# Performance work log

Measured on AMD Instinct MI355X. Metric: run time of the kernel, lower is better.

Reference implementation:

```python
import jax, jax.numpy as jnp
import numpy as np

DIM = 128      # dim
NC = 50000     # number of code nodes
NE = 100000    # number of hyperedges (visits)
T = 800000     # total flattened (code, edge) incidences
GAMMA = 0.5


def setup_inputs() -> dict:
    key = jax.random.key(0)
    ks = jax.random.split(key, 18)
    d = DIM
    s = 1.0 / np.sqrt(d)
    return {
        "H_e": jax.random.normal(ks[0], (NE, d), jnp.float32),
        "H_c": jax.random.normal(ks[1], (NC, d), jnp.float32),
        "timestamps": jax.random.uniform(ks[2], (NE,), jnp.float32),
        "W_e": jax.random.normal(ks[3], (d, d), jnp.float32) * s,
        "be_lin": jax.random.normal(ks[4], (d,), jnp.float32) * s,
        "b_e": jnp.zeros((d,), jnp.float32),
        "W_c": jax.random.normal(ks[5], (d, d), jnp.float32) * s,
        "bc_lin": jax.random.normal(ks[6], (d,), jnp.float32) * s,
        "b_c": jnp.zeros((d,), jnp.float32),
        "W_t": jax.random.normal(ks[7], (d, d), jnp.float32) * s,
        "b_t": jax.random.normal(ks[8], (d,), jnp.float32) * s,
        "W_g": jax.random.normal(ks[9], (d, d), jnp.float32) * s,
        "b_g": jax.random.normal(ks[10], (d,), jnp.float32) * s,
        "omega": jax.random.normal(ks[11], (d // 2,), jnp.float32),
        "W_t2v": jax.random.normal(ks[12], (d, d), jnp.float32) * s,
        "b_t2v": jax.random.normal(ks[13], (d,), jnp.float32) * s,
        "edge_ids": jax.random.randint(ks[14], (T,), 0, NE, jnp.int32),
        "seg_ids": jnp.sort(jax.random.randint(ks[15], (T,), 0, NC, jnp.int32)),
    }


def reference(H_e, H_c, timestamps, W_e, be_lin, b_e, W_c, bc_lin, b_c,
              W_t, b_t, W_g, b_g, omega, W_t2v, b_t2v, edge_ids, seg_ids):
    n_codes = H_c.shape[0]
    # --- gather variable-length neighbor sets (flattened segments) ---
    hes = H_e[edge_ids]                      # [T, d]
    hcs = H_c[seg_ids]                       # [T, d]
    tes = timestamps[edge_ids]               # [T]
    # --- Time2Vec ---
    tw = tes[:, None] * omega                # [T, d//2]
    t2v = jnp.concatenate([jnp.cos(tw), jnp.sin(tw)], axis=-1) @ W_t2v + b_t2v  # [T, d]
    # --- score: <proj_e * proj_c, sigmoid(linear_t(alpha_e))> ---
    proj_e = hes @ W_e + be_lin + b_e        # [T, d]
    proj_c = hcs @ W_c + bc_lin + b_c        # [T, d]
    gate = jax.nn.sigmoid(t2v @ W_t + b_t)   # [T, d]
    scores = jnp.sum(proj_e * proj_c * gate, axis=-1)  # [T]
    # --- segment softmax over each code's neighbor set ---
    smax = jax.ops.segment_max(scores, seg_ids, num_segments=n_codes)
    smax = jnp.where(jnp.isfinite(smax), smax, 0.0)
    ex = jnp.exp(scores - smax[seg_ids])
    denom = jax.ops.segment_sum(ex, seg_ids, num_segments=n_codes)
    attn = ex / jnp.maximum(denom, 1e-30)[seg_ids]      # [T]
    # --- weighted aggregate of g(h_e), scatter back to codes ---
    msg = attn[:, None] * (hes @ W_g + b_g)             # [T, d]
    agg = jax.ops.segment_sum(msg, seg_ids, num_segments=n_codes)  # [Nc, d]
    cnt = jax.ops.segment_sum(jnp.ones_like(scores), seg_ids, num_segments=n_codes)
    has_edge = (cnt > 0)[:, None]
    return jnp.where(has_edge, GAMMA * agg + (1.0 - GAMMA) * H_c, H_c)
```

## Files before the change

kernel.cpp:

```cpp
#include <hip/hip_runtime.h>
#include <math.h>

#define DIM   128
#define NC_   50000
#define NE_   100000
#define T_    800000

typedef __attribute__((ext_vector_type(8))) _Float16 f16x8;
typedef __attribute__((ext_vector_type(2))) _Float16 f16x2;
typedef __attribute__((ext_vector_type(4))) float f32x4;

__device__ __forceinline__ float sigmoidf_(float x) {
    return 1.f / (1.f + __expf(-x));
}

__device__ __forceinline__ float dot2f(f16x2 a, f16x2 b, float c) {
#if defined(__has_builtin) && __has_builtin(__builtin_amdgcn_fdot2)
    return __builtin_amdgcn_fdot2(a, b, c, false);
#else
    return c + (float)a[0] * (float)b[0] + (float)a[1] * (float)b[1];
#endif
}

__global__ __launch_bounds__(128)
void k_combine(const float* __restrict__ W_t2v, const float* __restrict__ W_t,
               const float* __restrict__ b_t2v, const float* __restrict__ b_t,
               float* __restrict__ W_tt, float* __restrict__ b_tt) {
    const int i = blockIdx.x, j = threadIdx.x;
    float acc = 0.f;
    if (i < DIM) {
        for (int k = 0; k < DIM; ++k) acc = fmaf(W_t2v[i*DIM+k], W_t[k*DIM+j], acc);
        W_tt[i*DIM+j] = acc;
    } else {
        for (int k = 0; k < DIM; ++k) acc = fmaf(b_t2v[k], W_t[k*DIM+j], acc);
        b_tt[j] = acc + b_t[j];
    }
}

__global__ __launch_bounds__(64)
void k_pack(const float* __restrict__ s0, const float* __restrict__ s1,
            const float* __restrict__ s2, const float* __restrict__ s3,
            _Float16* __restrict__ d0, _Float16* __restrict__ d1,
            _Float16* __restrict__ d2, _Float16* __restrict__ d3) {
    const float* srcs[4] = {s0, s1, s2, s3};
    _Float16* dsts[4] = {d0, d1, d2, d3};
    const float* src = srcs[blockIdx.y];
    _Float16* dst = dsts[blockIdx.y];
    const int b = blockIdx.x;
    const int nt = b >> 2, kb = b & 3;
    const int lane = threadIdx.x;
    const int n  = nt * 16 + (lane & 15);
    const int k0 = kb * 32 + 8 * (lane >> 4);
    const size_t off = ((size_t)(nt * 4 + kb) * 64 + lane) * 8;
    #pragma unroll
    for (int e = 0; e < 8; ++e)
        dst[off + e] = (_Float16)src[(size_t)(k0 + e) * DIM + n];
}

__global__ __launch_bounds__(256)
void k_starts(const int* __restrict__ seg, int* __restrict__ start) {
    int t = blockIdx.x * 256 + threadIdx.x;
    if (t > T_) return;
    if (t < T_) {
        int s  = seg[t];
        int sp = (t > 0) ? seg[t-1] : -1;
        for (int c = sp + 1; c <= s; ++c) start[c] = t;
    } else {
        int sp = seg[T_-1];
        for (int c = sp + 1; c <= NC_; ++c) start[c] = T_;
    }
}

__device__ __forceinline__ void split8h(const float* xs, f16x8* hi, f16x8* lo) {
    #pragma unroll
    for (int e = 0; e < 8; ++e) {
        _Float16 h = (_Float16)xs[e];
        (*hi)[e] = h;
        (*lo)[e] = (_Float16)(xs[e] - (float)h);
    }
}

__device__ __forceinline__ void stage_lds(_Float16* lds, const _Float16* __restrict__ g) {
    const int tid = threadIdx.x;
    #pragma unroll
    for (int i = 0; i < 8; ++i)
        ((uint4*)lds)[tid + i * 256] = ((const uint4*)g)[tid + i * 256];
}

__device__ __forceinline__ void mfma2(f16x8 ahi, f16x8 alo, const _Float16* lds_bp,
                                      f32x4* acc) {
    f16x8 b = *(const f16x8*)lds_bp;
    *acc = __builtin_amdgcn_mfma_f32_16x16x32_f16(ahi, b, *acc, 0, 0, 0);
    *acc = __builtin_amdgcn_mfma_f32_16x16x32_f16(alo, b, *acc, 0, 0, 0);
}

__global__ __launch_bounds__(256)
void k_edge(const float* __restrict__ H_e, const float* __restrict__ ts,
            const _Float16* __restrict__ packWe, const _Float16* __restrict__ packWtt,
            const float* __restrict__ be_lin, const float* __restrict__ b_e,
            const float* __restrict__ b_tt, const float* __restrict__ omega,
            _Float16* __restrict__ u16, _Float16* __restrict__ He16) {
    __shared__ __align__(16) _Float16 ldsW[16384];
    const int tid  = threadIdx.x;
    const int lane = tid & 63;
    const int q    = lane & 15, g = lane >> 4;
    const int brow = blockIdx.x * 64 + (tid >> 6) * 16;
    const int arow = brow + q;
    const bool valid = arow < NE_;
    const float* ap = H_e + (size_t)(valid ? arow : 0) * DIM;
    const float te  = valid ? ts[arow] : 0.f;

    stage_lds(ldsW, packWe);

    f32x4 accU[8], accG[8];
    #pragma unroll
    for (int i = 0; i < 8; ++i) {
        accU[i] = (f32x4){0.f, 0.f, 0.f, 0.f};
        accG[i] = (f32x4){0.f, 0.f, 0.f, 0.f};
    }
    __syncthreads();

    #pragma unroll
    for (int kb = 0; kb < 4; ++kb) {
        const int k0 = kb * 32 + 8 * g;
        float xs[8];
        if (valid) {
            float4 x0 = *(const float4*)(ap + k0);
            float4 x1 = *(const float4*)(ap + k0 + 4);
            xs[0]=x0.x; xs[1]=x0.y; xs[2]=x0.z; xs[3]=x0.w;
            xs[4]=x1.x; xs[5]=x1.y; xs[6]=x1.z; xs[7]=x1.w;
        } else {
            #pragma unroll
            for (int e = 0; e < 8; ++e) xs[e] = 0.f;
        }
        f16x8 ahi, alo;
        split8h(xs, &ahi, &alo);
        if (valid) *(f16x8*)&He16[(size_t)arow * DIM + k0] = ahi;
        #pragma unroll
        for (int nt = 0; nt < 8; ++nt)
            mfma2(ahi, alo, &ldsW[((nt * 4 + kb) * 64 + lane) * 8], &accU[nt]);
    }

    __syncthreads();
    stage_lds(ldsW, packWtt);
    __syncthreads();

    #pragma unroll
    for (int kb = 0; kb < 4; ++kb) {
        const int k0 = kb * 32 + 8 * g;
        float ys[8];
        #pragma unroll
        for (int e = 0; e < 8; ++e) {
            const int k = k0 + e;
            float x = te * omega[k & 63];
            float s, c;
            __sincosf(x, &s, &c);
            ys[e] = (k < 64) ? c : s;
        }
        f16x8 thi, tlo;
        split8h(ys, &thi, &tlo);
        #pragma unroll
        for (int nt = 0; nt < 8; ++nt)
            mfma2(thi, tlo, &ldsW[((nt * 4 + kb) * 64 + lane) * 8], &accG[nt]);
    }

    #pragma unroll
    for (int nt = 0; nt < 8; ++nt) {
        const int col = nt * 16 + q;
        const float bu = be_lin[col] + b_e[col];
        const float bg = b_tt[col];
        #pragma unroll
        for (int reg = 0; reg < 4; ++reg) {
            const int e = brow + 4 * g + reg;
            if (e < NE_) {
                float val = (accU[nt][reg] + bu) * sigmoidf_(accG[nt][reg] + bg);
                u16[(size_t)e * DIM + col] = (_Float16)val;
            }
        }
    }
}

__global__ __launch_bounds__(256)
void k_code(const float* __restrict__ H_c, const _Float16* __restrict__ packWc,
            const float* __restrict__ bc_lin, const float* __restrict__ b_c,
            _Float16* __restrict__ pc16) {
    __shared__ __align__(16) _Float16 ldsW[16384];
    const int tid  = threadIdx.x;
    const int lane = tid & 63;
    const int q    = lane & 15, g = lane >> 4;
    const int brow = blockIdx.x * 64 + (tid >> 6) * 16;
    const int arow = brow + q;
    const bool valid = arow < NC_;
    const float* ap = H_c + (size_t)(valid ? arow : 0) * DIM;

    stage_lds(ldsW, packWc);

    f32x4 acc[8];
    #pragma unroll
    for (int i = 0; i < 8; ++i) acc[i] = (f32x4){0.f, 0.f, 0.f, 0.f};
    __syncthreads();

    #pragma unroll
    for (int kb = 0; kb < 4; ++kb) {
        const int k0 = kb * 32 + 8 * g;
        float xs[8];
        if (valid) {
            float4 x0 = *(const float4*)(ap + k0);
            float4 x1 = *(const float4*)(ap + k0 + 4);
            xs[0]=x0.x; xs[1]=x0.y; xs[2]=x0.z; xs[3]=x0.w;
            xs[4]=x1.x; xs[5]=x1.y; xs[6]=x1.z; xs[7]=x1.w;
        } else {
            #pragma unroll
            for (int e = 0; e < 8; ++e) xs[e] = 0.f;
        }
        f16x8 ahi, alo;
        split8h(xs, &ahi, &alo);
        #pragma unroll
        for (int nt = 0; nt < 8; ++nt)
            mfma2(ahi, alo, &ldsW[((nt * 4 + kb) * 64 + lane) * 8], &acc[nt]);
    }

    #pragma unroll
    for (int nt = 0; nt < 8; ++nt) {
        const int col = nt * 16 + q;
        const float bc = bc_lin[col] + b_c[col];
        #pragma unroll
        for (int reg = 0; reg < 4; ++reg) {
            const int c = brow + 4 * g + reg;
            if (c < NC_) pc16[(size_t)c * DIM + col] = (_Float16)(acc[nt][reg] + bc);
        }
    }
}

__global__ __launch_bounds__(256)
void k_seg(const _Float16* __restrict__ u16, _Float16* __restrict__ pc16,
           const _Float16* __restrict__ He16, const int* __restrict__ edge_ids,
           const int* __restrict__ start) {
    const int lane = threadIdx.x & 63;
    const int c = blockIdx.x * 4 + (threadIdx.x >> 6);
    if (c >= NC_) return;
    const int lo = start[c], hi = start[c + 1];
    const int g = lane >> 3;
    const int q = lane & 7;
    const int j0 = q * 16;

    union { uint4 r[2]; f16x2 h2[8]; } pcu;
    pcu.r[0] = *(const uint4*)&pc16[(size_t)c * DIM + j0];
    pcu.r[1] = *(const uint4*)&pc16[(size_t)c * DIM + j0 + 8];

    float M = -INFINITY, S = 0.f;
    float acc[16];
    #pragma unroll
    for (int i = 0; i < 16; ++i) acc[i] = 0.f;

    for (int base = lo; base < hi; base += 64) {
        const int n = min(64, hi - base);
        const int eid = (base + lane < hi) ? edge_ids[base + lane] : 0;
        const int niter = (n + 7) >> 3;
        float msc = -INFINITY;

        for (int jj = 0; jj < niter; ++jj) {
            const int s = 8 * jj + g;
            const int e = __shfl(eid, s);
            float p = 0.f;
            if (s < n) {
                union { uint4 r[2]; f16x2 h2[8]; } uu;
                const _Float16* up = &u16[(size_t)e * DIM + j0];
                uu.r[0] = *(const uint4*)up;
                uu.r[1] = *(const uint4*)(up + 8);
                #pragma unroll
                for (int i = 0; i < 8; ++i) p = dot2f(uu.h2[i], pcu.h2[i], p);
            }
            p += __shfl_xor(p, 1);
            p += __shfl_xor(p, 2);
            p += __shfl_xor(p, 4);
            if (q == jj && s < n) msc = p;
        }

        float cm = msc;
        #pragma unroll
        for (int off = 32; off; off >>= 1) cm = fmaxf(cm, __shfl_xor(cm, off));
        const float nM = fmaxf(M, cm);
        const float scale = __expf(M - nM);
        const float pi = __expf(msc - nM);
        float ss = pi;
        #pragma unroll
        for (int off = 32; off; off >>= 1) ss += __shfl_xor(ss, off);
        S = S * scale + ss;
        #pragma unroll
        for (int i = 0; i < 16; ++i) acc[i] *= scale;
        M = nM;

        for (int jj = 0; jj < niter; ++jj) {
            const int s = 8 * jj + g;
            const int e = __shfl(eid, s);
            const float p = __shfl(pi, 8 * g + jj);
            if (s < n) {
                union { uint4 r[2]; f16x8 h8[2]; } hh;
                const _Float16* hp = &He16[(size_t)e * DIM + j0];
                hh.r[0] = *(const uint4*)hp;
                hh.r[1] = *(const uint4*)(hp + 8);
                #pragma unroll
                for (int i = 0; i < 8; ++i) {
                    acc[i]     = fmaf(p, (float)hh.h8[0][i], acc[i]);
                    acc[8 + i] = fmaf(p, (float)hh.h8[1][i], acc[8 + i]);
                }
            }
        }
    }

    #pragma unroll
    for (int off = 8; off <= 32; off <<= 1) {
        #pragma unroll
        for (int i = 0; i < 16; ++i) acc[i] += __shfl_xor(acc[i], off);
    }

    if (g == 0) {
        const float inv = (hi > lo) ? 1.f / fmaxf(S, 1e-30f) : 0.f;
        union { uint4 r[2]; _Float16 h[16]; } o;
        #pragma unroll
        for (int i = 0; i < 16; ++i) o.h[i] = (_Float16)(acc[i] * inv);
        *(uint4*)&pc16[(size_t)c * DIM + j0]     = o.r[0];
        *(uint4*)&pc16[(size_t)c * DIM + j0 + 8] = o.r[1];
    }
}

__global__ __launch_bounds__(256)
void k_out(const _Float16* __restrict__ v16, const _Float16* __restrict__ packWg,
           const float* __restrict__ b_g, const float* __restrict__ H_c,
           const int* __restrict__ start, float* __restrict__ out) {
    __shared__ __align__(16) _Float16 ldsW[16384];
    const int tid  = threadIdx.x;
    const int lane = tid & 63;
    const int q    = lane & 15, g = lane >> 4;
    const int brow = blockIdx.x * 64 + (tid >> 6) * 16;
    const int arow = brow + q;
    const bool valid = arow < NC_;
    const _Float16* ap = v16 + (size_t)(valid ? arow : 0) * DIM;

    stage_lds(ldsW, packWg);

    f32x4 acc[8];
    #pragma unroll
    for (int i = 0; i < 8; ++i) acc[i] = (f32x4){0.f, 0.f, 0.f, 0.f};
    __syncthreads();

    #pragma unroll
    for (int kb = 0; kb < 4; ++kb) {
        const int k0 = kb * 32 + 8 * g;
        f16x8 a;
        if (valid) {
            a = *(const f16x8*)(ap + k0);
        } else {
            #pragma unroll
            for (int e = 0; e < 8; ++e) a[e] = (_Float16)0.f;
        }
        #pragma unroll
        for (int nt = 0; nt < 8; ++nt) {
            f16x8 b = *(const f16x8*)&ldsW[((nt * 4 + kb) * 64 + lane) * 8];
            acc[nt] = __builtin_amdgcn_mfma_f32_16x16x32_f16(a, b, acc[nt], 0, 0, 0);
        }
    }

    #pragma unroll
    for (int reg = 0; reg < 4; ++reg) {
        const int c = brow + 4 * g + reg;
        if (c >= NC_) continue;
        const bool has = start[c + 1] > start[c];
        #pragma unroll
        for (int nt = 0; nt < 8; ++nt) {
            const int col = nt * 16 + q;
            const float hc = H_c[(size_t)c * DIM + col];
            float o = has ? 0.5f * (acc[nt][reg] + b_g[col]) + 0.5f * hc : hc;
            out[(size_t)c * DIM + col] = o;
        }
    }
}

extern "C" void kernel_launch(void* const* d_in, const int* in_sizes, int n_in,
                              void* d_out, int out_size, void* d_ws, size_t ws_size,
                              hipStream_t stream) {
    const float* H_e    = (const float*)d_in[0];
    const float* H_c    = (const float*)d_in[1];
    const float* ts     = (const float*)d_in[2];
    const float* W_e    = (const float*)d_in[3];
    const float* be_lin = (const float*)d_in[4];
    const float* b_e    = (const float*)d_in[5];
    const float* W_c    = (const float*)d_in[6];
    const float* bc_lin = (const float*)d_in[7];
    const float* b_c    = (const float*)d_in[8];
    const float* W_t    = (const float*)d_in[9];
    const float* b_t    = (const float*)d_in[10];
    const float* W_g    = (const float*)d_in[11];
    const float* b_g    = (const float*)d_in[12];
    const float* omega  = (const float*)d_in[13];
    const float* W_t2v  = (const float*)d_in[14];
    const float* b_t2v  = (const float*)d_in[15];
    const int* edge_ids = (const int*)d_in[16];
    const int* seg_ids  = (const int*)d_in[17];
    float* out = (float*)d_out;

    char* w = (char*)d_ws;
    _Float16* u16  = (_Float16*)w; w += (size_t)NE_ * DIM * sizeof(_Float16);
    _Float16* He16 = (_Float16*)w; w += (size_t)NE_ * DIM * sizeof(_Float16);
    _Float16* pc16 = (_Float16*)w; w += (size_t)NC_ * DIM * sizeof(_Float16);
    int* start  = (int*)w;    w += (((size_t)(NC_ + 1) * sizeof(int)) + 255) & ~(size_t)255;
    float* W_tt = (float*)w;  w += (size_t)DIM * DIM * sizeof(float);
    float* b_tt = (float*)w;  w += 1024;
    _Float16* packWe  = (_Float16*)w; w += 16384 * sizeof(_Float16);
    _Float16* packWtt = (_Float16*)w; w += 16384 * sizeof(_Float16);
    _Float16* packWc  = (_Float16*)w; w += 16384 * sizeof(_Float16);
    _Float16* packWg  = (_Float16*)w; w += 16384 * sizeof(_Float16);
    if ((size_t)(w - (char*)d_ws) > ws_size) return;

    k_combine<<<dim3(DIM + 1), dim3(128), 0, stream>>>(W_t2v, W_t, b_t2v, b_t, W_tt, b_tt);
    k_pack<<<dim3(32, 4), dim3(64), 0, stream>>>(W_e, W_tt, W_c, W_g,
                                                 packWe, packWtt, packWc, packWg);
    k_starts<<<dim3((T_ + 1 + 255) / 256), dim3(256), 0, stream>>>(seg_ids, start);
    k_edge<<<dim3((NE_ + 63) / 64), dim3(256), 0, stream>>>(H_e, ts, packWe, packWtt,
                                                            be_lin, b_e, b_tt, omega,
                                                            u16, He16);
    k_code<<<dim3((NC_ + 63) / 64), dim3(256), 0, stream>>>(H_c, packWc, bc_lin, b_c, pc16);
    k_seg<<<dim3((NC_ + 3) / 4), dim3(256), 0, stream>>>(u16, pc16, He16, edge_ids, start);
    k_out<<<dim3((NC_ + 63) / 64), dim3(256), 0, stream>>>(pc16, packWg, b_g, H_c, start, out);
}
```

Measured before the change: 142.5 us.

## Make edge projection kernel persistent with both weight matrices resident in LDS

The edge kernel now stages both the W_e and combined time-gate weight packs into LDS once per block (64 KB). A fixed grid of 512 blocks then loops over 64-row tiles, so the weight staging and bias/omega loads are paid once per block instead of once per tile. The two GEMM loops are also fused into one k-loop. The larger LDS footprint lowers the number of resident blocks per CU, and fewer blocks may reduce latency hiding.

```diff
diff --git a/kernel.cpp b/kernel.cpp
--- a/kernel.cpp
+++ b/kernel.cpp
@@ -5,6 +5,7 @@
 #define NC_   50000
 #define NE_   100000
 #define T_    800000
+#define NTILE_E ((NE_ + 63) / 64)
 
 typedef __attribute__((ext_vector_type(8))) _Float16 f16x8;
 typedef __attribute__((ext_vector_type(2))) _Float16 f16x2;
@@ -100,81 +101,91 @@
             const float* __restrict__ be_lin, const float* __restrict__ b_e,
             const float* __restrict__ b_tt, const float* __restrict__ omega,
             _Float16* __restrict__ u16, _Float16* __restrict__ He16) {
-    __shared__ __align__(16) _Float16 ldsW[16384];
+    __shared__ __align__(16) _Float16 ldsW[32768];
     const int tid  = threadIdx.x;
     const int lane = tid & 63;
     const int q    = lane & 15, g = lane >> 4;
-    const int brow = blockIdx.x * 64 + (tid >> 6) * 16;
-    const int arow = brow + q;
-    const bool valid = arow < NE_;
-    const float* ap = H_e + (size_t)(valid ? arow : 0) * DIM;
-    const float te  = valid ? ts[arow] : 0.f;
+    const int wv   = tid >> 6;
 
     stage_lds(ldsW, packWe);
-
-    f32x4 accU[8], accG[8];
-    #pragma unroll
-    for (int i = 0; i < 8; ++i) {
-        accU[i] = (f32x4){0.f, 0.f, 0.f, 0.f};
-        accG[i] = (f32x4){0.f, 0.f, 0.f, 0.f};
-    }
-    __syncthreads();
-
+    stage_lds(ldsW + 16384, packWtt);
+
+    float bu[8], bg[8];
+    #pragma unroll
+    for (int nt = 0; nt < 8; ++nt) {
+        const int col = nt * 16 + q;
+        bu[nt] = be_lin[col] + b_e[col];
+        bg[nt] = b_tt[col];
+    }
+    float om[4][8];
     #pragma unroll
     for (int kb = 0; kb < 4; ++kb) {
         const int k0 = kb * 32 + 8 * g;
-        float xs[8];
-        if (valid) {
-            float4 x0 = *(const float4*)(ap + k0);
-            float4 x1 = *(const float4*)(ap + k0 + 4);
-            xs[0]=x0.x; xs[1]=x0.y; xs[2]=x0.z; xs[3]=x0.w;
-            xs[4]=x1.x; xs[5]=x1.y; xs[6]=x1.z; xs[7]=x1.w;
-        } else {
-            #pragma unroll
-            for (int e = 0; e < 8; ++e) xs[e] = 0.f;
-        }
-        f16x8 ahi, alo;
-        split8h(xs, &ahi, &alo);
-        if (valid) *(f16x8*)&He16[(size_t)arow * DIM + k0] = ahi;
-        #pragma unroll
-        for (int nt = 0; nt < 8; ++nt)
-            mfma2(ahi, alo, &ldsW[((nt * 4 + kb) * 64 + lane) * 8], &accU[nt]);
-    }
-
+        #pragma unroll
+        for (int e = 0; e < 8; ++e) om[kb][e] = omega[(k0 + e) & 63];
+    }
     __syncthreads();
-    stage_lds(ldsW, packWtt);
-    __syncthreads();
-
-    #pragma unroll
-    for (int kb = 0; kb < 4; ++kb) {
-        const int k0 = kb * 32 + 8 * g;
-        float ys[8];
-        #pragma unroll
-        for (int e = 0; e < 8; ++e) {
-            const int k = k0 + e;
-            float x = te * omega[k & 63];
-            float s, c;
-            __sincosf(x, &s, &c);
-            ys[e] = (k < 64) ? c : s;
-        }
-        f16x8 thi, tlo;
-        split8h(ys, &thi, &tlo);
-        #pragma unroll
-        for (int nt = 0; nt < 8; ++nt)
-            mfma2(thi, tlo, &ldsW[((nt * 4 + kb) * 64 + lane) * 8], &accG[nt]);
-    }
-
-    #pragma unroll
-    for (int nt = 0; nt < 8; ++nt) {
-        const int col = nt * 16 + q;
-        const float bu = be_lin[col] + b_e[col];
-        const float bg = b_tt[col];
-        #pragma unroll
-        for (int reg = 0; reg < 4; ++reg) {
-            const int e = brow + 4 * g + reg;
-            if (e < NE_) {
-                float val = (accU[nt][reg] + bu) * sigmoidf_(accG[nt][reg] + bg);
-                u16[(size_t)e * DIM + col] = (_Float16)val;
+
+    for (int tile = blockIdx.x; tile < NTILE_E; tile += gridDim.x) {
+        const int brow = tile * 64 + wv * 16;
+        const int arow = brow + q;
+        const bool valid = arow < NE_;
+        const float* ap = H_e + (size_t)(valid ? arow : 0) * DIM;
+        const float te  = valid ? ts[arow] : 0.f;
+
+        f32x4 accU[8], accG[8];
+        #pragma unroll
+        for (int i = 0; i < 8; ++i) {
+            accU[i] = (f32x4){0.f, 0.f, 0.f, 0.f};
+            accG[i] = (f32x4){0.f, 0.f, 0.f, 0.f};
+        }
+
+        #pragma unroll
+        for (int kb = 0; kb < 4; ++kb) {
+            const int k0 = kb * 32 + 8 * g;
+
+            float xs[8];
+            if (valid) {
+                float4 x0 = *(const float4*)(ap + k0);
+                float4 x1 = *(const float4*)(ap + k0 + 4);
+                xs[0]=x0.x; xs[1]=x0.y; xs[2]=x0.z; xs[3]=x0.w;
+                xs[4]=x1.x; xs[5]=x1.y; xs[6]=x1.z; xs[7]=x1.w;
+            } else {
+                #pragma unroll
+                for (int e = 0; e < 8; ++e) xs[e] = 0.f;
+            }
+            f16x8 ahi, alo;
+            split8h(xs, &ahi, &alo);
+            if (valid) *(f16x8*)&He16[(size_t)arow * DIM + k0] = ahi;
+            #pragma unroll
+            for (int nt = 0; nt < 8; ++nt)
+                mfma2(ahi, alo, &ldsW[((nt * 4 + kb) * 64 + lane) * 8], &accU[nt]);
+
+            float ys[8];
+            #pragma unroll
+            for (int e = 0; e < 8; ++e) {
+                float x = te * om[kb][e];
+                float s, c;
+                __sincosf(x, &s, &c);
+                ys[e] = (k0 + e < 64) ? c : s;
+            }
+            f16x8 thi, tlo;
+            split8h(ys, &thi, &tlo);
+            #pragma unroll
+            for (int nt = 0; nt < 8; ++nt)
+                mfma2(thi, tlo, &ldsW[16384 + ((nt * 4 + kb) * 64 + lane) * 8], &accG[nt]);
+        }
+
+        #pragma unroll
+        for (int nt = 0; nt < 8; ++nt) {
+            const int col = nt * 16 + q;
+            #pragma unroll
+            for (int reg = 0; reg < 4; ++reg) {
+                const int e = brow + 4 * g + reg;
+                if (e < NE_) {
+                    float val = (accU[nt][reg] + bu[nt]) * sigmoidf_(accG[nt][reg] + bg[nt]);
+                    u16[(size_t)e * DIM + col] = (_Float16)val;
+                }
             }
         }
     }
@@ -417,9 +428,8 @@
     k_pack<<<dim3(32, 4), dim3(64), 0, stream>>>(W_e, W_tt, W_c, W_g,
                                                  packWe, packWtt, packWc, packWg);
     k_starts<<<dim3((T_ + 1 + 255) / 256), dim3(256), 0, stream>>>(seg_ids, start);
-    k_edge<<<dim3((NE_ + 63) / 64), dim3(256), 0, stream>>>(H_e, ts, packWe, packWtt,
-                                                            be_lin, b_e, b_tt, omega,
-                                                            u16, He16);
+    k_edge<<<dim3(512), dim3(256), 0, stream>>>(H_e, ts, packWe, packWtt,
+                                                be_lin, b_e, b_tt, omega, u16, He16);
     k_code<<<dim3((NC_ + 63) / 64), dim3(256), 0, stream>>>(H_c, packWc, bc_lin, b_c, pc16);
     k_seg<<<dim3((NC_ + 3) / 4), dim3(256), 0, stream>>>(u16, pc16, He16, edge_ids, start);
     k_out<<<dim3((NC_ + 63) / 64), dim3(256), 0, stream>>>(pc16, packWg, b_g, H_c, start, out);
```

Result: slower. 147.3 us (+3.4%).

## Merge edge and code projection kernels and stage outputs through LDS

Applied to the files above, without the earlier changes.

Combines the edge projection/gating kernel and the code projection kernel into one launch, with block index selecting the branch, so both run concurrently and one launch plus its tail is removed. Outputs are also staged in LDS with a padded stride and written back as 16-byte row-contiguous stores instead of scattered 2-byte stores. This adds extra barriers and LDS traffic per block in exchange for coalesced global writes.

```diff
diff --git a/kernel.cpp b/kernel.cpp
--- a/kernel.cpp
+++ b/kernel.cpp
@@ -5,6 +5,8 @@
 #define NC_   50000
 #define NE_   100000
 #define T_    800000
+#define NTILE_E ((NE_ + 63) / 64)
+#define NTILE_C ((NC_ + 63) / 64)
 
 typedef __attribute__((ext_vector_type(8))) _Float16 f16x8;
 typedef __attribute__((ext_vector_type(2))) _Float16 f16x2;
@@ -94,140 +96,168 @@
     *acc = __builtin_amdgcn_mfma_f32_16x16x32_f16(alo, b, *acc, 0, 0, 0);
 }
 
+#define TSTRIDE 136
+
 __global__ __launch_bounds__(256)
-void k_edge(const float* __restrict__ H_e, const float* __restrict__ ts,
+void k_main(const float* __restrict__ H_e, const float* __restrict__ ts,
             const _Float16* __restrict__ packWe, const _Float16* __restrict__ packWtt,
+            const _Float16* __restrict__ packWc,
             const float* __restrict__ be_lin, const float* __restrict__ b_e,
-            const float* __restrict__ b_tt, const float* __restrict__ omega,
-            _Float16* __restrict__ u16, _Float16* __restrict__ He16) {
-    __shared__ __align__(16) _Float16 ldsW[16384];
-    const int tid  = threadIdx.x;
-    const int lane = tid & 63;
-    const int q    = lane & 15, g = lane >> 4;
-    const int brow = blockIdx.x * 64 + (tid >> 6) * 16;
-    const int arow = brow + q;
-    const bool valid = arow < NE_;
-    const float* ap = H_e + (size_t)(valid ? arow : 0) * DIM;
-    const float te  = valid ? ts[arow] : 0.f;
-
-    stage_lds(ldsW, packWe);
-
-    f32x4 accU[8], accG[8];
-    #pragma unroll
-    for (int i = 0; i < 8; ++i) {
-        accU[i] = (f32x4){0.f, 0.f, 0.f, 0.f};
-        accG[i] = (f32x4){0.f, 0.f, 0.f, 0.f};
-    }
-    __syncthreads();
-
-    #pragma unroll
-    for (int kb = 0; kb < 4; ++kb) {
-        const int k0 = kb * 32 + 8 * g;
-        float xs[8];
-        if (valid) {
-            float4 x0 = *(const float4*)(ap + k0);
-            float4 x1 = *(const float4*)(ap + k0 + 4);
-            xs[0]=x0.x; xs[1]=x0.y; xs[2]=x0.z; xs[3]=x0.w;
-            xs[4]=x1.x; xs[5]=x1.y; xs[6]=x1.z; xs[7]=x1.w;
-        } else {
-            #pragma unroll
-            for (int e = 0; e < 8; ++e) xs[e] = 0.f;
-        }
-        f16x8 ahi, alo;
-        split8h(xs, &ahi, &alo);
-        if (valid) *(f16x8*)&He16[(size_t)arow * DIM + k0] = ahi;
-        #pragma unroll
-        for (int nt = 0; nt < 8; ++nt)
-            mfma2(ahi, alo, &ldsW[((nt * 4 + kb) * 64 + lane) * 8], &accU[nt]);
-    }
-
-    __syncthreads();
-    stage_lds(ldsW, packWtt);
-    __syncthreads();
-
-    #pragma unroll
-    for (int kb = 0; kb < 4; ++kb) {
-        const int k0 = kb * 32 + 8 * g;
-        float ys[8];
-        #pragma unroll
-        for (int e = 0; e < 8; ++e) {
-            const int k = k0 + e;
-            float x = te * omega[k & 63];
-            float s, c;
-            __sincosf(x, &s, &c);
-            ys[e] = (k < 64) ? c : s;
-        }
-        f16x8 thi, tlo;
-        split8h(ys, &thi, &tlo);
-        #pragma unroll
-        for (int nt = 0; nt < 8; ++nt)
-            mfma2(thi, tlo, &ldsW[((nt * 4 + kb) * 64 + lane) * 8], &accG[nt]);
-    }
-
-    #pragma unroll
-    for (int nt = 0; nt < 8; ++nt) {
-        const int col = nt * 16 + q;
-        const float bu = be_lin[col] + b_e[col];
-        const float bg = b_tt[col];
-        #pragma unroll
-        for (int reg = 0; reg < 4; ++reg) {
-            const int e = brow + 4 * g + reg;
-            if (e < NE_) {
-                float val = (accU[nt][reg] + bu) * sigmoidf_(accG[nt][reg] + bg);
-                u16[(size_t)e * DIM + col] = (_Float16)val;
-            }
-        }
-    }
-}
-
-__global__ __launch_bounds__(256)
-void k_code(const float* __restrict__ H_c, const _Float16* __restrict__ packWc,
+            const float* __restrict__ b_tt,
             const float* __restrict__ bc_lin, const float* __restrict__ b_c,
+            const float* __restrict__ omega, const float* __restrict__ H_c,
+            _Float16* __restrict__ u16, _Float16* __restrict__ He16,
             _Float16* __restrict__ pc16) {
     __shared__ __align__(16) _Float16 ldsW[16384];
     const int tid  = threadIdx.x;
     const int lane = tid & 63;
     const int q    = lane & 15, g = lane >> 4;
-    const int brow = blockIdx.x * 64 + (tid >> 6) * 16;
-    const int arow = brow + q;
-    const bool valid = arow < NC_;
-    const float* ap = H_c + (size_t)(valid ? arow : 0) * DIM;
-
-    stage_lds(ldsW, packWc);
-
-    f32x4 acc[8];
-    #pragma unroll
-    for (int i = 0; i < 8; ++i) acc[i] = (f32x4){0.f, 0.f, 0.f, 0.f};
-    __syncthreads();
-
-    #pragma unroll
-    for (int kb = 0; kb < 4; ++kb) {
-        const int k0 = kb * 32 + 8 * g;
-        float xs[8];
-        if (valid) {
-            float4 x0 = *(const float4*)(ap + k0);
-            float4 x1 = *(const float4*)(ap + k0 + 4);
-            xs[0]=x0.x; xs[1]=x0.y; xs[2]=x0.z; xs[3]=x0.w;
-            xs[4]=x1.x; xs[5]=x1.y; xs[6]=x1.z; xs[7]=x1.w;
-        } else {
-            #pragma unroll
-            for (int e = 0; e < 8; ++e) xs[e] = 0.f;
-        }
-        f16x8 ahi, alo;
-        split8h(xs, &ahi, &alo);
-        #pragma unroll
-        for (int nt = 0; nt < 8; ++nt)
-            mfma2(ahi, alo, &ldsW[((nt * 4 + kb) * 64 + lane) * 8], &acc[nt]);
-    }
-
-    #pragma unroll
-    for (int nt = 0; nt < 8; ++nt) {
-        const int col = nt * 16 + q;
-        const float bc = bc_lin[col] + b_c[col];
-        #pragma unroll
-        for (int reg = 0; reg < 4; ++reg) {
-            const int c = brow + 4 * g + reg;
-            if (c < NC_) pc16[(size_t)c * DIM + col] = (_Float16)(acc[nt][reg] + bc);
+    const int wv   = tid >> 6;
+
+    if (blockIdx.x < NTILE_E) {
+        const int tile = blockIdx.x;
+        const int brow = tile * 64 + wv * 16;
+        const int arow = brow + q;
+        const bool valid = arow < NE_;
+        const float* ap = H_e + (size_t)(valid ? arow : 0) * DIM;
+        const float te  = valid ? ts[arow] : 0.f;
+
+        stage_lds(ldsW, packWe);
+
+        f32x4 accU[8], accG[8];
+        #pragma unroll
+        for (int i = 0; i < 8; ++i) {
+            accU[i] = (f32x4){0.f, 0.f, 0.f, 0.f};
+            accG[i] = (f32x4){0.f, 0.f, 0.f, 0.f};
+        }
+        __syncthreads();
+
+        #pragma unroll
+        for (int kb = 0; kb < 4; ++kb) {
+            const int k0 = kb * 32 + 8 * g;
+            float xs[8];
+            if (valid) {
+                float4 x0 = *(const float4*)(ap + k0);
+                float4 x1 = *(const float4*)(ap + k0 + 4);
+                xs[0]=x0.x; xs[1]=x0.y; xs[2]=x0.z; xs[3]=x0.w;
+                xs[4]=x1.x; xs[5]=x1.y; xs[6]=x1.z; xs[7]=x1.w;
+            } else {
+                #pragma unroll
+                for (int e = 0; e < 8; ++e) xs[e] = 0.f;
+            }
+            f16x8 ahi, alo;
+            split8h(xs, &ahi, &alo);
+            if (valid) *(f16x8*)&He16[(size_t)arow * DIM + k0] = ahi;
+            #pragma unroll
+            for (int nt = 0; nt < 8; ++nt)
+                mfma2(ahi, alo, &ldsW[((nt * 4 + kb) * 64 + lane) * 8], &accU[nt]);
+        }
+
+        __syncthreads();
+        stage_lds(ldsW, packWtt);
+        __syncthreads();
+
+        #pragma unroll
+        for (int kb = 0; kb < 4; ++kb) {
+            const int k0 = kb * 32 + 8 * g;
+            float ys[8];
+            #pragma unroll
+            for (int e = 0; e < 8; ++e) {
+                const int k = k0 + e;
+                float x = te * omega[k & 63];
+                float s, c;
+                __sincosf(x, &s, &c);
+                ys[e] = (k < 64) ? c : s;
+            }
+            f16x8 thi, tlo;
+            split8h(ys, &thi, &tlo);
+            #pragma unroll
+            for (int nt = 0; nt < 8; ++nt)
+                mfma2(thi, tlo, &ldsW[((nt * 4 + kb) * 64 + lane) * 8], &accG[nt]);
+        }
+
+        __syncthreads();
+        #pragma unroll
+        for (int nt = 0; nt < 8; ++nt) {
+            const int col = nt * 16 + q;
+            const float bu = be_lin[col] + b_e[col];
+            const float bg = b_tt[col];
+            #pragma unroll
+            for (int reg = 0; reg < 4; ++reg) {
+                float val = (accU[nt][reg] + bu) * sigmoidf_(accG[nt][reg] + bg);
+                ldsW[(wv * 16 + 4 * g + reg) * TSTRIDE + col] = (_Float16)val;
+            }
+        }
+        __syncthreads();
+        {
+            const int row = tid >> 2;
+            const int c0  = (tid & 3) * 32;
+            const int er  = tile * 64 + row;
+            if (er < NE_) {
+                const _Float16* sp = &ldsW[row * TSTRIDE + c0];
+                uint4* dst = (uint4*)&u16[(size_t)er * DIM + c0];
+                dst[0] = *(const uint4*)(sp + 0);
+                dst[1] = *(const uint4*)(sp + 8);
+                dst[2] = *(const uint4*)(sp + 16);
+                dst[3] = *(const uint4*)(sp + 24);
+            }
+        }
+    } else {
+        const int tile = blockIdx.x - NTILE_E;
+        const int brow = tile * 64 + wv * 16;
+        const int arow = brow + q;
+        const bool valid = arow < NC_;
+        const float* ap = H_c + (size_t)(valid ? arow : 0) * DIM;
+
+        stage_lds(ldsW, packWc);
+
+        f32x4 acc[8];
+        #pragma unroll
+        for (int i = 0; i < 8; ++i) acc[i] = (f32x4){0.f, 0.f, 0.f, 0.f};
+        __syncthreads();
+
+        #pragma unroll
+        for (int kb = 0; kb < 4; ++kb) {
+            const int k0 = kb * 32 + 8 * g;
+            float xs[8];
+            if (valid) {
+                float4 x0 = *(const float4*)(ap + k0);
+                float4 x1 = *(const float4*)(ap + k0 + 4);
+                xs[0]=x0.x; xs[1]=x0.y; xs[2]=x0.z; xs[3]=x0.w;
+                xs[4]=x1.x; xs[5]=x1.y; xs[6]=x1.z; xs[7]=x1.w;
+            } else {
+                #pragma unroll
+                for (int e = 0; e < 8; ++e) xs[e] = 0.f;
+            }
+            f16x8 ahi, alo;
+            split8h(xs, &ahi, &alo);
+            #pragma unroll
+            for (int nt = 0; nt < 8; ++nt)
+                mfma2(ahi, alo, &ldsW[((nt * 4 + kb) * 64 + lane) * 8], &acc[nt]);
+        }
+
+        __syncthreads();
+        #pragma unroll
+        for (int nt = 0; nt < 8; ++nt) {
+            const int col = nt * 16 + q;
+            const float bc = bc_lin[col] + b_c[col];
+            #pragma unroll
+            for (int reg = 0; reg < 4; ++reg)
+                ldsW[(wv * 16 + 4 * g + reg) * TSTRIDE + col] = (_Float16)(acc[nt][reg] + bc);
+        }
+        __syncthreads();
+        {
+            const int row = tid >> 2;
+            const int c0  = (tid & 3) * 32;
+            const int cr  = tile * 64 + row;
+            if (cr < NC_) {
+                const _Float16* sp = &ldsW[row * TSTRIDE + c0];
+                uint4* dst = (uint4*)&pc16[(size_t)cr * DIM + c0];
+                dst[0] = *(const uint4*)(sp + 0);
+                dst[1] = *(const uint4*)(sp + 8);
+                dst[2] = *(const uint4*)(sp + 16);
+                dst[3] = *(const uint4*)(sp + 24);
+            }
         }
     }
 }
@@ -417,10 +447,9 @@
     k_pack<<<dim3(32, 4), dim3(64), 0, stream>>>(W_e, W_tt, W_c, W_g,
                                                  packWe, packWtt, packWc, packWg);
     k_starts<<<dim3((T_ + 1 + 255) / 256), dim3(256), 0, stream>>>(seg_ids, start);
-    k_edge<<<dim3((NE_ + 63) / 64), dim3(256), 0, stream>>>(H_e, ts, packWe, packWtt,
-                                                            be_lin, b_e, b_tt, omega,
-                                                            u16, He16);
-    k_code<<<dim3((NC_ + 63) / 64), dim3(256), 0, stream>>>(H_c, packWc, bc_lin, b_c, pc16);
+    k_main<<<dim3(NTILE_E + NTILE_C), dim3(256), 0, stream>>>(
+        H_e, ts, packWe, packWtt, packWc, be_lin, b_e, b_tt, bc_lin, b_c,
+        omega, H_c, u16, He16, pc16);
     k_seg<<<dim3((NC_ + 3) / 4), dim3(256), 0, stream>>>(u16, pc16, He16, edge_ids, start);
     k_out<<<dim3((NC_ + 63) / 64), dim3(256), 0, stream>>>(pc16, packWg, b_g, H_c, start, out);
 }
```

Measured after the change: 137.5 us. 3.5% less time.
